# Kernel optimization log

Hardware: AMD Instinct MI355X
Metric: run time of the kernel (lower is better)

The kernel has to match this reference:

```python
import jax, jax.numpy as jnp
import numpy as np

N_NODES = 100000
N_EDGES = 1600000
MUL = 32            # channel multiplicity for every irrep
INV_SQRT_MUL = 1.0 / np.sqrt(32.0)
# path constants: wigner-3j norms (1/sqrt3 for 0x1->1 and 1x1->0, 1/sqrt6 for 1x1->1)
# combined with fan-in path normalization (fan=32 for 0e out, fan=64 for 1o out, 2 paths)
C_DOT = 1.0 / np.sqrt(3.0 * 32.0)
C_SCL = 1.0 / np.sqrt(3.0 * 64.0)
C_CRS = 1.0 / np.sqrt(6.0 * 64.0)


def setup_inputs() -> dict:
    key = jax.random.key(0)
    ks = jax.random.split(key, 12)
    x = jax.random.normal(ks[0], (N_NODES, 128), jnp.float32)
    pos = jax.random.normal(ks[1], (N_NODES, 3), jnp.float32)
    edge_index = jax.random.randint(ks[2], (2, N_EDGES), 0, N_NODES, jnp.int32)
    # o3.Linear(32x0e+32x1o -> 32x0e+32x0e+32x1o): per-irrep channel mixing
    W_node_s = jax.random.normal(ks[3], (32, 64), jnp.float32)   # 0e -> (scalars|gates)
    W_node_v = jax.random.normal(ks[4], (32, 32), jnp.float32)   # 1o -> 1o
    # FullyConnectedTensorProduct(32x0e+32x1o, 1x1o -> 32x0e+32x1o): 3 CG paths
    W_tp_d = jax.random.normal(ks[5], (32, 32), jnp.float32)     # 1o x 1o -> 0e (dot)
    W_tp_s = jax.random.normal(ks[6], (32, 32), jnp.float32)     # 0e x 1o -> 1o
    W_tp_c = jax.random.normal(ks[7], (32, 32), jnp.float32)     # 1o x 1o -> 1o (cross)
    # o3.Linear(32x0e+32x1o -> 32x0e+32x1o)
    W_msg_s = jax.random.normal(ks[8], (32, 32), jnp.float32)
    W_msg_v = jax.random.normal(ks[9], (32, 32), jnp.float32)
    ln_gamma = jnp.ones((128,), jnp.float32)
    ln_beta = jnp.zeros((128,), jnp.float32)
    return {"x": x, "pos": pos, "edge_index": edge_index,
            "W_node_s": W_node_s, "W_node_v": W_node_v,
            "W_tp_d": W_tp_d, "W_tp_s": W_tp_s, "W_tp_c": W_tp_c,
            "W_msg_s": W_msg_s, "W_msg_v": W_msg_v,
            "ln_gamma": ln_gamma, "ln_beta": ln_beta}


def reference(x, pos, edge_index, W_node_s, W_node_v, W_tp_d, W_tp_s, W_tp_c,
              W_msg_s, W_msg_v, ln_gamma, ln_beta):
    N = x.shape[0]
    row, col = edge_index[0], edge_index[1]
    # split node irreps: 32 scalars (0e) | 32 vectors (1o) of dim 3
    s = x[:, :32]                       # [N,32]
    v = x[:, 32:].reshape(-1, 32, 3)    # [N,32,3]
    # lin_node (equivariant linear, path-normalized by 1/sqrt(fan_in)=1/sqrt(32))
    h_s = (s @ W_node_s) * INV_SQRT_MUL                          # [N,64]
    h_v = jnp.einsum('nid,ij->njd', v, W_node_v) * INV_SQRT_MUL  # [N,32,3]
    # Gate: relu scalars, sigmoid gates multiply the gated vectors
    sc = jax.nn.relu(h_s[:, :32])                                # [N,32]
    hv = h_v * jax.nn.sigmoid(h_s[:, 32:])[:, :, None]           # [N,32,3]
    # spherical harmonics l=1, component norm: sqrt(3)*unit vec in e3nn (y,z,x) order
    rel = pos[col] - pos[row]                                    # [E,3]
    unit = rel / jnp.sqrt(jnp.sum(rel * rel, -1, keepdims=True) + 1e-12)
    u = jnp.sqrt(3.0) * unit[:, (1, 2, 0)]                       # [E,3]
    # gather source-node features per edge
    sj = sc[col]                                                 # [E,32]
    vj = hv[col]                                                 # [E,32,3]
    # CG tensor product paths
    dot = jnp.einsum('eid,ed->ei', vj, u)                        # 1o x 1o -> 0e
    crs = jnp.cross(vj, u[:, None, :])                           # 1o x 1o -> 1o
    m0 = (dot @ W_tp_d) * C_DOT                                  # [E,32]
    m1 = (sj @ W_tp_s)[:, :, None] * u[:, None, :] * C_SCL \
         + jnp.einsum('eid,ik->ekd', crs, W_tp_c) * C_CRS        # [E,32,3]
    m = jnp.concatenate([m0, m1.reshape(-1, 96)], -1)            # [E,128]
    # scatter-mean over destination nodes (row)
    deg = jax.ops.segment_sum(jnp.ones_like(row, jnp.float32), row,
                              num_segments=N).clip(1.0)
    mi = jax.ops.segment_sum(m, row, num_segments=N) / deg[:, None]
    # lin_msg
    ms = (mi[:, :32] @ W_msg_s) * INV_SQRT_MUL
    mv = jnp.einsum('nid,ij->njd', mi[:, 32:].reshape(-1, 32, 3),
                    W_msg_v) * INV_SQRT_MUL
    o = jnp.concatenate([ms, mv.reshape(-1, 96)], -1)            # [N,128]
    # LayerNorm over 128 dims (as in the original, affine)
    mu = o.mean(-1, keepdims=True)
    var = o.var(-1, keepdims=True)
    o = (o - mu) / jnp.sqrt(var + 1e-5) * ln_gamma + ln_beta
    return x + o
```

## Files before the change

### kernel.cpp

```cpp
#include <hip/hip_runtime.h>
#include <math.h>


static constexpr float INV_SQRT_MUL = 0.17677669529663687f;
static constexpr float C_DOT = 0.10206207261596575f;
static constexpr float C_SCL = 0.07216878364870322f;
static constexpr float C_CRS = 0.05103103630798288f;
static constexpr float SQRT3 = 1.7320508075688772f;
static constexpr int MAXDEG = 48;
static constexpr int SCAT_B = 2048;
static constexpr int CNT_WORDS = 8 * 16384;

#define WS_ALIGN(x) (((x) + 255) & ~(size_t)255)
#define CIDX(r) ((((r) & 7) << 14) | ((r) >> 3))

__device__ __forceinline__ unsigned short f2bf(float v) {
    unsigned int b = __float_as_uint(v);
    b += 0x7FFFu + ((b >> 16) & 1u);
    return (unsigned short)(b >> 16);
}
__device__ __forceinline__ float bf2f(unsigned short u) {
    return __uint_as_float(((unsigned int)u) << 16);
}

__global__ __launch_bounds__(1024)
void fuse_zero(const float* __restrict__ Wns, const float* __restrict__ Wnv,
               const float* __restrict__ Wtpd, const float* __restrict__ Wtps,
               const float* __restrict__ Wtpc, const float* __restrict__ Wms,
               const float* __restrict__ Wmv, float* __restrict__ Wall,
               int* __restrict__ cnt) {
    int t = threadIdx.x;
    if (blockIdx.x == 0) {
        int i = t >> 5, j = t & 31;
        float a = 0.f, b = 0.f, c = 0.f;
#pragma unroll
        for (int k = 0; k < 32; ++k) {
            a += Wtpd[i * 32 + k] * Wms[k * 32 + j];
            b += Wtps[i * 32 + k] * Wmv[k * 32 + j];
            c += Wtpc[i * 32 + k] * Wmv[k * 32 + j];
        }
        Wall[t]        = a * (C_DOT * INV_SQRT_MUL);
        Wall[1024 + t] = b * (C_SCL * INV_SQRT_MUL);
        Wall[2048 + t] = c * (C_CRS * INV_SQRT_MUL);
        int i2 = t >> 5, k2 = t & 31;
        Wall[3072 + t]        = Wns[k2 * 64 + i2];
        Wall[3072 + 1024 + t] = Wns[k2 * 64 + 32 + i2];
        Wall[5120 + t]        = Wnv[k2 * 32 + i2];
    } else {
        int i = (blockIdx.x - 1) * 1024 + t;
        if (i < CNT_WORDS) cnt[i] = 0;
    }
}

__global__ __launch_bounds__(256)
void scatter(const int* __restrict__ eidx, int* __restrict__ cnt,
             int* __restrict__ slots, int E) {
    int shard = blockIdx.x & 7;
    int tid = (blockIdx.x >> 3) * 256 + threadIdx.x;
    const int SSTRIDE = (SCAT_B / 8) * 256;
    int Q = E >> 2;
    const int4* r4p = (const int4*)eidx;
    const int4* c4p = (const int4*)(eidx + E);
    for (int q = tid; q < Q; q += SSTRIDE) {
        int4 R = r4p[q];
        bool any = ((R.x & 7) == shard) | ((R.y & 7) == shard) |
                   ((R.z & 7) == shard) | ((R.w & 7) == shard);
        if (!any) continue;
        int4 C = c4p[q];
        int rr[4] = {R.x, R.y, R.z, R.w};
        int cc[4] = {C.x, C.y, C.z, C.w};
#pragma unroll
        for (int k = 0; k < 4; ++k) {
            if ((rr[k] & 7) == shard) {
                int p = atomicAdd(&cnt[CIDX(rr[k])], 1);
                if (p < MAXDEG) slots[(size_t)rr[k] * MAXDEG + p] = cc[k];
            }
        }
    }
    for (int e = (Q << 2) + tid; e < E; e += SSTRIDE) {
        int r = eidx[e];
        if ((r & 7) == shard) {
            int c = eidx[E + e];
            int p = atomicAdd(&cnt[CIDX(r)], 1);
            if (p < MAXDEG) slots[(size_t)r * MAXDEG + p] = c;
        }
    }
}

__global__ __launch_bounds__(64)
void node_feat(const float* __restrict__ x, const float* __restrict__ WT,
               ushort4* __restrict__ feat4, int N) {
    __shared__ float buf[64 * 100];
    int l = threadIdx.x;
    int nt = (N + 63) >> 6;
    const float* WnsT = WT;
    const float* WnvT = WT + 2048;
    for (int tile = blockIdx.x; tile < nt; tile += gridDim.x) {
        int B = tile << 6;
        {
            int r0 = l >> 3, cw = (l & 7) * 4;
            for (int j = 0; j < 8; ++j) {
                int row = j * 8 + r0;
                int node = B + row;
                float4 v = make_float4(0.f, 0.f, 0.f, 0.f);
                if (node < N) v = *(const float4*)(x + (size_t)node * 128 + cw);
                *(float4*)(buf + row * 36 + cw) = v;
            }
        }
        __syncthreads();
        float xsv[32];
        {
            const float4* rp = (const float4*)(buf + l * 36);
#pragma unroll
            for (int j = 0; j < 8; ++j) {
                float4 q = rp[j];
                xsv[4 * j] = q.x; xsv[4 * j + 1] = q.y;
                xsv[4 * j + 2] = q.z; xsv[4 * j + 3] = q.w;
            }
        }
        unsigned int scp[16];
        float sig[32];
#pragma unroll 2
        for (int i = 0; i < 32; ++i) {
            float a = 0.f, g = 0.f;
#pragma unroll
            for (int k = 0; k < 32; ++k) {
                a += xsv[k] * WnsT[i * 32 + k];
                g += xsv[k] * WnsT[(32 + i) * 32 + k];
            }
            a = fmaxf(a * INV_SQRT_MUL, 0.f);
            float s = 1.f / (1.f + __expf(-g * INV_SQRT_MUL));
            unsigned short s16 = f2bf(a);
            if ((i & 1) == 0) scp[i >> 1] = s16;
            else scp[i >> 1] |= ((unsigned int)s16) << 16;
            sig[i] = s * INV_SQRT_MUL;
        }
        __syncthreads();
        {
            int r0 = l >> 3, cw = (l & 7) * 4;
            for (int j = 0; j < 24; ++j) {
                int third = j >> 3, j8 = j & 7;
                int row = j8 * 8 + r0;
                int node = B + row;
                int w0 = 32 + third * 32 + cw;
                float4 v = make_float4(0.f, 0.f, 0.f, 0.f);
                if (node < N) v = *(const float4*)(x + (size_t)node * 128 + w0);
                *(float4*)(buf + row * 100 + (w0 - 32)) = v;
            }
        }
        __syncthreads();
        float xv[96];
        {
            const float4* rp = (const float4*)(buf + l * 100);
#pragma unroll
            for (int j = 0; j < 24; ++j) {
                float4 q = rp[j];
                xv[4 * j] = q.x; xv[4 * j + 1] = q.y;
                xv[4 * j + 2] = q.z; xv[4 * j + 3] = q.w;
            }
        }
        int node = B + l;
        bool live = (node < N);
#pragma unroll 2
        for (int i = 0; i < 32; ++i) {
            float o0 = 0.f, o1 = 0.f, o2 = 0.f;
#pragma unroll
            for (int k = 0; k < 32; ++k) {
                float wv = WnvT[i * 32 + k];
                o0 += xv[3 * k + 0] * wv;
                o1 += xv[3 * k + 1] * wv;
                o2 += xv[3 * k + 2] * wv;
            }
            float s = sig[i];
            unsigned int scw = scp[i >> 1];
            ushort4 pk;
            pk.x = (unsigned short)((i & 1) ? (scw >> 16) : (scw & 0xFFFFu));
            pk.y = f2bf(o0 * s); pk.z = f2bf(o1 * s); pk.w = f2bf(o2 * s);
            if (live) feat4[(size_t)node * 32 + i] = pk;
        }
        __syncthreads();
    }
}

template <int U>
__device__ __forceinline__ void agg_chunk(const float4* __restrict__ curow, int j,
    const ushort4* __restrict__ feat4, int lane,
    float& D, float& S0, float& S1, float& S2,
    float& C0, float& C1, float& C2) {
    float4 q[U];
    ushort4 f[U];
#pragma unroll
    for (int k = 0; k < U; ++k) q[k] = curow[j + k];
#pragma unroll
    for (int k = 0; k < U; ++k)
        f[k] = feat4[(size_t)__float_as_int(q[k].w) * 32 + lane];
#pragma unroll
    for (int k = 0; k < U; ++k) {
        float u0 = q[k].x, u1 = q[k].y, u2 = q[k].z;
        float sj = bf2f(f[k].x);
        float h0 = bf2f(f[k].y), h1 = bf2f(f[k].z), h2 = bf2f(f[k].w);
        D  += h0 * u0 + h1 * u1 + h2 * u2;
        S0 += sj * u0; S1 += sj * u1; S2 += sj * u2;
        C0 += h1 * u2 - h2 * u1;
        C1 += h2 * u0 - h0 * u2;
        C2 += h0 * u1 - h1 * u0;
    }
}

__global__ __launch_bounds__(256)
void agg(const float* __restrict__ x, const float* __restrict__ pos,
         const ushort4* __restrict__ feat4, const int* __restrict__ cnt,
         const int* __restrict__ slots, const float* __restrict__ Wall,
         const float* __restrict__ gamma, const float* __restrict__ beta,
         float* __restrict__ out, int N) {
    int t = threadIdx.x;
    int hw = t >> 5, lane = t & 31;
    int n = blockIdx.x * 8 + hw;
    bool live = (n < N);
    int nn = live ? n : 0;

    __shared__ float4 cu[8][MAXDEG];
    __shared__ float4 finA[8][32];
    __shared__ float4 finB[8][32];

    int deg = live ? cnt[CIDX(n)] : 0;
    int c = min(deg, MAXDEG);

    float prx = pos[nn * 3 + 0], pry = pos[nn * 3 + 1], prz = pos[nn * 3 + 2];

    if (lane < c) {
        int col = slots[(size_t)nn * MAXDEG + lane];
        float rx = pos[col * 3 + 0] - prx, ry = pos[col * 3 + 1] - pry, rz = pos[col * 3 + 2] - prz;
        float inv = rsqrtf(rx * rx + ry * ry + rz * rz + 1e-12f) * SQRT3;
        cu[hw][lane] = make_float4(ry * inv, rz * inv, rx * inv, __int_as_float(col));
    }
    if (lane + 32 < c) {
        int col = slots[(size_t)nn * MAXDEG + 32 + lane];
        float rx = pos[col * 3 + 0] - prx, ry = pos[col * 3 + 1] - pry, rz = pos[col * 3 + 2] - prz;
        float inv = rsqrtf(rx * rx + ry * ry + rz * rz + 1e-12f) * SQRT3;
        cu[hw][32 + lane] = make_float4(ry * inv, rz * inv, rx * inv, __int_as_float(col));
    }
    __syncthreads();

    float D = 0.f, S0 = 0.f, S1 = 0.f, S2 = 0.f, C0 = 0.f, C1 = 0.f, C2 = 0.f;
    const float4* curow = cu[hw];
    int j = 0;
    for (; j + 8 <= c; j += 8) agg_chunk<8>(curow, j, feat4, lane, D, S0, S1, S2, C0, C1, C2);
    if (j + 4 <= c) { agg_chunk<4>(curow, j, feat4, lane, D, S0, S1, S2, C0, C1, C2); j += 4; }
    for (; j < c; ++j) agg_chunk<1>(curow, j, feat4, lane, D, S0, S1, S2, C0, C1, C2);

    finA[hw][lane] = make_float4(D, S0, S1, S2);
    finB[hw][lane] = make_float4(C0, C1, C2, 0.f);
    __syncthreads();

    float invdeg = 1.0f / (float)((deg > 0) ? deg : 1);
    float a0 = 0.f, aV0 = 0.f, aV1 = 0.f, aV2 = 0.f;
#pragma unroll 8
    for (int i = 0; i < 32; ++i) {
        float4 a = finA[hw][i];
        float4 b = finB[hw][i];
        float wd = Wall[i * 32 + lane];
        float ws = Wall[1024 + i * 32 + lane];
        float wc = Wall[2048 + i * 32 + lane];
        a0  += a.x * wd;
        aV0 += a.y * ws + b.x * wc;
        aV1 += a.z * ws + b.y * wc;
        aV2 += a.w * ws + b.z * wc;
    }
    float vd = a0 * invdeg;
    float v0 = aV0 * invdeg, v1 = aV1 * invdeg, v2 = aV2 * invdeg;

    float s1 = vd + v0 + v1 + v2;
    float s2 = vd * vd + v0 * v0 + v1 * v1 + v2 * v2;
#pragma unroll
    for (int m = 16; m >= 1; m >>= 1) {
        s1 += __shfl_xor(s1, m);
        s2 += __shfl_xor(s2, m);
    }
    float mu = s1 * (1.f / 128.f);
    float var = s2 * (1.f / 128.f) - mu * mu;
    float rstd = rsqrtf(var + 1e-5f);

    if (live) {
        size_t base = (size_t)n * 128;
        int chv = 32 + lane * 3;
        float xv0 = __builtin_nontemporal_load(&x[base + lane]);
        float xa  = __builtin_nontemporal_load(&x[base + chv + 0]);
        float xb  = __builtin_nontemporal_load(&x[base + chv + 1]);
        float xc  = __builtin_nontemporal_load(&x[base + chv + 2]);
        __builtin_nontemporal_store(xv0 + (vd - mu) * rstd * gamma[lane] + beta[lane], &out[base + lane]);
        __builtin_nontemporal_store(xa + (v0 - mu) * rstd * gamma[chv + 0] + beta[chv + 0], &out[base + chv + 0]);
        __builtin_nontemporal_store(xb + (v1 - mu) * rstd * gamma[chv + 1] + beta[chv + 1], &out[base + chv + 1]);
        __builtin_nontemporal_store(xc + (v2 - mu) * rstd * gamma[chv + 2] + beta[chv + 2], &out[base + chv + 2]);
    }
}

extern "C" void kernel_launch(void* const* d_in, const int* in_sizes, int n_in,
                              void* d_out, int out_size, void* d_ws, size_t ws_size,
                              hipStream_t stream) {
    const float* x     = (const float*)d_in[0];
    const float* pos   = (const float*)d_in[1];
    const int*   eidx  = (const int*)d_in[2];
    const float* Wns   = (const float*)d_in[3];
    const float* Wnv   = (const float*)d_in[4];
    const float* Wtpd  = (const float*)d_in[5];
    const float* Wtps  = (const float*)d_in[6];
    const float* Wtpc  = (const float*)d_in[7];
    const float* Wms   = (const float*)d_in[8];
    const float* Wmv   = (const float*)d_in[9];
    const float* gamma = (const float*)d_in[10];
    const float* beta  = (const float*)d_in[11];
    float* out = (float*)d_out;

    int N = in_sizes[0] / 128;
    int E = in_sizes[2] / 2;

    char* ws = (char*)d_ws;
    size_t off = 0;
    unsigned short* feat = (unsigned short*)(ws + off); off += WS_ALIGN((size_t)N * 128 * 2);
    int*   cnt  = (int*)(ws + off);   off += WS_ALIGN((size_t)CNT_WORDS * 4);
    float* Wall = (float*)(ws + off); off += WS_ALIGN(6144 * 4);
    int*   slots = (int*)(ws + off);

    int zb = 1 + (CNT_WORDS + 1023) / 1024;
    fuse_zero<<<zb, 1024, 0, stream>>>(Wns, Wnv, Wtpd, Wtps, Wtpc, Wms, Wmv, Wall, cnt);
    scatter<<<SCAT_B, 256, 0, stream>>>(eidx, cnt, slots, E);
    int nt = (N + 63) >> 6;
    node_feat<<<nt, 64, 0, stream>>>(x, Wall + 3072, (ushort4*)feat, N);
    agg<<<(N + 7) / 8, 256, 0, stream>>>(x, pos, (const ushort4*)feat, cnt, slots, Wall, gamma, beta, out, N);
}
```

Baseline: 437.5 us.

## Restructure agg to one node per wave with split edges, batch node_feat waves

```diff
diff --git a/kernel.cpp b/kernel.cpp
--- a/kernel.cpp
+++ b/kernel.cpp
@@ -24,32 +24,26 @@
 }
 
 __global__ __launch_bounds__(1024)
-void fuse_zero(const float* __restrict__ Wns, const float* __restrict__ Wnv,
-               const float* __restrict__ Wtpd, const float* __restrict__ Wtps,
-               const float* __restrict__ Wtpc, const float* __restrict__ Wms,
-               const float* __restrict__ Wmv, float* __restrict__ Wall,
-               int* __restrict__ cnt) {
+void fuse_w(const float* __restrict__ Wns, const float* __restrict__ Wnv,
+            const float* __restrict__ Wtpd, const float* __restrict__ Wtps,
+            const float* __restrict__ Wtpc, const float* __restrict__ Wms,
+            const float* __restrict__ Wmv, float* __restrict__ Wall) {
     int t = threadIdx.x;
-    if (blockIdx.x == 0) {
-        int i = t >> 5, j = t & 31;
-        float a = 0.f, b = 0.f, c = 0.f;
-#pragma unroll
-        for (int k = 0; k < 32; ++k) {
-            a += Wtpd[i * 32 + k] * Wms[k * 32 + j];
-            b += Wtps[i * 32 + k] * Wmv[k * 32 + j];
-            c += Wtpc[i * 32 + k] * Wmv[k * 32 + j];
-        }
-        Wall[t]        = a * (C_DOT * INV_SQRT_MUL);
-        Wall[1024 + t] = b * (C_SCL * INV_SQRT_MUL);
-        Wall[2048 + t] = c * (C_CRS * INV_SQRT_MUL);
-        int i2 = t >> 5, k2 = t & 31;
-        Wall[3072 + t]        = Wns[k2 * 64 + i2];
-        Wall[3072 + 1024 + t] = Wns[k2 * 64 + 32 + i2];
-        Wall[5120 + t]        = Wnv[k2 * 32 + i2];
-    } else {
-        int i = (blockIdx.x - 1) * 1024 + t;
-        if (i < CNT_WORDS) cnt[i] = 0;
-    }
+    int i = t >> 5, j = t & 31;
+    float a = 0.f, b = 0.f, c = 0.f;
+#pragma unroll
+    for (int k = 0; k < 32; ++k) {
+        a += Wtpd[i * 32 + k] * Wms[k * 32 + j];
+        b += Wtps[i * 32 + k] * Wmv[k * 32 + j];
+        c += Wtpc[i * 32 + k] * Wmv[k * 32 + j];
+    }
+    Wall[t]        = a * (C_DOT * INV_SQRT_MUL);
+    Wall[1024 + t] = b * (C_SCL * INV_SQRT_MUL);
+    Wall[2048 + t] = c * (C_CRS * INV_SQRT_MUL);
+    int i2 = t >> 5, k2 = t & 31;
+    Wall[3072 + t]        = Wns[k2 * 64 + i2];
+    Wall[3072 + 1024 + t] = Wns[k2 * 64 + 32 + i2];
+    Wall[5120 + t]        = Wnv[k2 * 32 + i2];
 }
 
 __global__ __launch_bounds__(256)
@@ -87,123 +81,83 @@
     }
 }
 
-__global__ __launch_bounds__(64)
+__global__ __launch_bounds__(256)
 void node_feat(const float* __restrict__ x, const float* __restrict__ WT,
                ushort4* __restrict__ feat4, int N) {
-    __shared__ float buf[64 * 100];
-    int l = threadIdx.x;
+    __shared__ float buf[4][64 * 36];
+    int t = threadIdx.x;
+    int wv = t >> 6, l = t & 63;
+    float* bw = buf[wv];
     int nt = (N + 63) >> 6;
+    int tile = blockIdx.x * 4 + wv;
+    if (tile >= nt) return;
+    int B = tile << 6;
+    int r0 = l >> 3, cw = (l & 7) << 2;
     const float* WnsT = WT;
     const float* WnvT = WT + 2048;
-    for (int tile = blockIdx.x; tile < nt; tile += gridDim.x) {
-        int B = tile << 6;
-        {
-            int r0 = l >> 3, cw = (l & 7) * 4;
-            for (int j = 0; j < 8; ++j) {
-                int row = j * 8 + r0;
-                int node = B + row;
-                float4 v = make_float4(0.f, 0.f, 0.f, 0.f);
-                if (node < N) v = *(const float4*)(x + (size_t)node * 128 + cw);
-                *(float4*)(buf + row * 36 + cw) = v;
-            }
-        }
-        __syncthreads();
-        float xsv[32];
-        {
-            const float4* rp = (const float4*)(buf + l * 36);
-#pragma unroll
-            for (int j = 0; j < 8; ++j) {
-                float4 q = rp[j];
-                xsv[4 * j] = q.x; xsv[4 * j + 1] = q.y;
-                xsv[4 * j + 2] = q.z; xsv[4 * j + 3] = q.w;
-            }
-        }
-        unsigned int scp[16];
-        float sig[32];
+
+    auto stage = [&](int w0) {
+#pragma unroll
+        for (int j = 0; j < 8; ++j) {
+            int row = j * 8 + r0;
+            int node = B + row;
+            float4 v = make_float4(0.f, 0.f, 0.f, 0.f);
+            if (node < N) v = *(const float4*)(x + (size_t)node * 128 + w0 + cw);
+            *(float4*)(bw + row * 36 + cw) = v;
+        }
+        __builtin_amdgcn_wave_barrier();
+    };
+    auto readrow = [&](float* dst) {
+        const float4* rp = (const float4*)(bw + l * 36);
+#pragma unroll
+        for (int j = 0; j < 8; ++j) {
+            float4 q = rp[j];
+            dst[4*j] = q.x; dst[4*j+1] = q.y; dst[4*j+2] = q.z; dst[4*j+3] = q.w;
+        }
+        __builtin_amdgcn_wave_barrier();
+    };
+
+    float xs[32];
+    stage(0); readrow(xs);
+    unsigned int scp[16];
+    float sig[32];
 #pragma unroll 2
-        for (int i = 0; i < 32; ++i) {
-            float a = 0.f, g = 0.f;
-#pragma unroll
-            for (int k = 0; k < 32; ++k) {
-                a += xsv[k] * WnsT[i * 32 + k];
-                g += xsv[k] * WnsT[(32 + i) * 32 + k];
-            }
-            a = fmaxf(a * INV_SQRT_MUL, 0.f);
-            float s = 1.f / (1.f + __expf(-g * INV_SQRT_MUL));
-            unsigned short s16 = f2bf(a);
-            if ((i & 1) == 0) scp[i >> 1] = s16;
-            else scp[i >> 1] |= ((unsigned int)s16) << 16;
-            sig[i] = s * INV_SQRT_MUL;
-        }
-        __syncthreads();
-        {
-            int r0 = l >> 3, cw = (l & 7) * 4;
-            for (int j = 0; j < 24; ++j) {
-                int third = j >> 3, j8 = j & 7;
-                int row = j8 * 8 + r0;
-                int node = B + row;
-                int w0 = 32 + third * 32 + cw;
-                float4 v = make_float4(0.f, 0.f, 0.f, 0.f);
-                if (node < N) v = *(const float4*)(x + (size_t)node * 128 + w0);
-                *(float4*)(buf + row * 100 + (w0 - 32)) = v;
-            }
-        }
-        __syncthreads();
-        float xv[96];
-        {
-            const float4* rp = (const float4*)(buf + l * 100);
-#pragma unroll
-            for (int j = 0; j < 24; ++j) {
-                float4 q = rp[j];
-                xv[4 * j] = q.x; xv[4 * j + 1] = q.y;
-                xv[4 * j + 2] = q.z; xv[4 * j + 3] = q.w;
-            }
-        }
-        int node = B + l;
-        bool live = (node < N);
+    for (int i = 0; i < 32; ++i) {
+        float a = 0.f, g = 0.f;
+#pragma unroll
+        for (int k = 0; k < 32; ++k) {
+            a += xs[k] * WnsT[i * 32 + k];
+            g += xs[k] * WnsT[(32 + i) * 32 + k];
+        }
+        a = fmaxf(a * INV_SQRT_MUL, 0.f);
+        float s = 1.f / (1.f + __expf(-g * INV_SQRT_MUL));
+        unsigned short s16 = f2bf(a);
+        if ((i & 1) == 0) scp[i >> 1] = s16;
+        else scp[i >> 1] |= ((unsigned int)s16) << 16;
+        sig[i] = s * INV_SQRT_MUL;
+    }
+    float xv[96];
+    stage(32); readrow(xv);
+    stage(64); readrow(xv + 32);
+    stage(96); readrow(xv + 64);
+    int node = B + l;
+    bool liv = (node < N);
 #pragma unroll 2
-        for (int i = 0; i < 32; ++i) {
-            float o0 = 0.f, o1 = 0.f, o2 = 0.f;
-#pragma unroll
-            for (int k = 0; k < 32; ++k) {
-                float wv = WnvT[i * 32 + k];
-                o0 += xv[3 * k + 0] * wv;
-                o1 += xv[3 * k + 1] * wv;
-                o2 += xv[3 * k + 2] * wv;
-            }
-            float s = sig[i];
-            unsigned int scw = scp[i >> 1];
-            ushort4 pk;
-            pk.x = (unsigned short)((i & 1) ? (scw >> 16) : (scw & 0xFFFFu));
-            pk.y = f2bf(o0 * s); pk.z = f2bf(o1 * s); pk.w = f2bf(o2 * s);
-            if (live) feat4[(size_t)node * 32 + i] = pk;
-        }
-        __syncthreads();
-    }
-}
-
-template <int U>
-__device__ __forceinline__ void agg_chunk(const float4* __restrict__ curow, int j,
-    const ushort4* __restrict__ feat4, int lane,
-    float& D, float& S0, float& S1, float& S2,
-    float& C0, float& C1, float& C2) {
-    float4 q[U];
-    ushort4 f[U];
-#pragma unroll
-    for (int k = 0; k < U; ++k) q[k] = curow[j + k];
-#pragma unroll
-    for (int k = 0; k < U; ++k)
-        f[k] = feat4[(size_t)__float_as_int(q[k].w) * 32 + lane];
-#pragma unroll
-    for (int k = 0; k < U; ++k) {
-        float u0 = q[k].x, u1 = q[k].y, u2 = q[k].z;
-        float sj = bf2f(f[k].x);
-        float h0 = bf2f(f[k].y), h1 = bf2f(f[k].z), h2 = bf2f(f[k].w);
-        D  += h0 * u0 + h1 * u1 + h2 * u2;
-        S0 += sj * u0; S1 += sj * u1; S2 += sj * u2;
-        C0 += h1 * u2 - h2 * u1;
-        C1 += h2 * u0 - h0 * u2;
-        C2 += h0 * u1 - h1 * u0;
+    for (int i = 0; i < 32; ++i) {
+        float o0 = 0.f, o1 = 0.f, o2 = 0.f;
+#pragma unroll
+        for (int k = 0; k < 32; ++k) {
+            float w = WnvT[i * 32 + k];
+            o0 += xv[3 * k + 0] * w;
+            o1 += xv[3 * k + 1] * w;
+            o2 += xv[3 * k + 2] * w;
+        }
+        float s = sig[i];
+        unsigned int scw = scp[i >> 1];
+        ushort4 pk;
+        pk.x = (unsigned short)((i & 1) ? (scw >> 16) : (scw & 0xFFFFu));
+        pk.y = f2bf(o0 * s); pk.z = f2bf(o1 * s); pk.w = f2bf(o2 * s);
+        if (liv) feat4[(size_t)node * 32 + i] = pk;
     }
 }
 
@@ -213,60 +167,89 @@
          const int* __restrict__ slots, const float* __restrict__ Wall,
          const float* __restrict__ gamma, const float* __restrict__ beta,
          float* __restrict__ out, int N) {
+    __shared__ float4 cu[4][MAXDEG];
+    __shared__ float4 finA[4][32];
+    __shared__ float4 finB[4][32];
     int t = threadIdx.x;
-    int hw = t >> 5, lane = t & 31;
-    int n = blockIdx.x * 8 + hw;
+    int wv = t >> 6, lane = t & 63;
+    int ch = lane & 31, slot = lane >> 5;
+    int n = blockIdx.x * 4 + wv;
     bool live = (n < N);
     int nn = live ? n : 0;
-
-    __shared__ float4 cu[8][MAXDEG];
-    __shared__ float4 finA[8][32];
-    __shared__ float4 finB[8][32];
-
-    int deg = live ? cnt[CIDX(n)] : 0;
+    int deg = cnt[CIDX(nn)];
+    if (!live) deg = 0;
     int c = min(deg, MAXDEG);
 
     float prx = pos[nn * 3 + 0], pry = pos[nn * 3 + 1], prz = pos[nn * 3 + 2];
-
     if (lane < c) {
         int col = slots[(size_t)nn * MAXDEG + lane];
         float rx = pos[col * 3 + 0] - prx, ry = pos[col * 3 + 1] - pry, rz = pos[col * 3 + 2] - prz;
         float inv = rsqrtf(rx * rx + ry * ry + rz * rz + 1e-12f) * SQRT3;
-        cu[hw][lane] = make_float4(ry * inv, rz * inv, rx * inv, __int_as_float(col));
-    }
-    if (lane + 32 < c) {
-        int col = slots[(size_t)nn * MAXDEG + 32 + lane];
-        float rx = pos[col * 3 + 0] - prx, ry = pos[col * 3 + 1] - pry, rz = pos[col * 3 + 2] - prz;
-        float inv = rsqrtf(rx * rx + ry * ry + rz * rz + 1e-12f) * SQRT3;
-        cu[hw][32 + lane] = make_float4(ry * inv, rz * inv, rx * inv, __int_as_float(col));
-    }
-    __syncthreads();
-
+        cu[wv][lane] = make_float4(ry * inv, rz * inv, rx * inv, __int_as_float(col << 8));
+    }
+    __builtin_amdgcn_wave_barrier();
+
+    const char* featB = (const char*)feat4;
+    unsigned int ch8 = (unsigned int)ch * 8u;
+    const float4* cuw = cu[wv];
     float D = 0.f, S0 = 0.f, S1 = 0.f, S2 = 0.f, C0 = 0.f, C1 = 0.f, C2 = 0.f;
-    const float4* curow = cu[hw];
-    int j = 0;
-    for (; j + 8 <= c; j += 8) agg_chunk<8>(curow, j, feat4, lane, D, S0, S1, S2, C0, C1, C2);
-    if (j + 4 <= c) { agg_chunk<4>(curow, j, feat4, lane, D, S0, S1, S2, C0, C1, C2); j += 4; }
-    for (; j < c; ++j) agg_chunk<1>(curow, j, feat4, lane, D, S0, S1, S2, C0, C1, C2);
-
-    finA[hw][lane] = make_float4(D, S0, S1, S2);
-    finB[hw][lane] = make_float4(C0, C1, C2, 0.f);
-    __syncthreads();
+
+    auto body = [&](const float4& q, const ushort4& f) {
+        float u0 = q.x, u1 = q.y, u2 = q.z;
+        float sj = bf2f(f.x);
+        float h0 = bf2f(f.y), h1 = bf2f(f.z), h2 = bf2f(f.w);
+        D  += h0 * u0 + h1 * u1 + h2 * u2;
+        S0 += sj * u0; S1 += sj * u1; S2 += sj * u2;
+        C0 += h1 * u2 - h2 * u1;
+        C1 += h2 * u0 - h0 * u2;
+        C2 += h0 * u1 - h1 * u0;
+    };
+
+    int jb = 0;
+    for (; jb + 8 <= c; jb += 8) {
+        float4 q[4]; ushort4 f[4];
+#pragma unroll
+        for (int k = 0; k < 4; ++k) q[k] = cuw[jb + 2 * k + slot];
+#pragma unroll
+        for (int k = 0; k < 4; ++k)
+            f[k] = *(const ushort4*)(featB + (__float_as_uint(q[k].w) + ch8));
+#pragma unroll
+        for (int k = 0; k < 4; ++k) body(q[k], f[k]);
+    }
+    for (int j = jb + slot; j < c; j += 2) {
+        float4 q = cuw[j];
+        ushort4 f = *(const ushort4*)(featB + (__float_as_uint(q.w) + ch8));
+        body(q, f);
+    }
+
+    D  += __shfl_xor(D, 32);
+    S0 += __shfl_xor(S0, 32); S1 += __shfl_xor(S1, 32); S2 += __shfl_xor(S2, 32);
+    C0 += __shfl_xor(C0, 32); C1 += __shfl_xor(C1, 32); C2 += __shfl_xor(C2, 32);
+    if (lane < 32) {
+        finA[wv][ch] = make_float4(D, S0, S1, S2);
+        finB[wv][ch] = make_float4(C0, C1, C2, 0.f);
+    }
+    __builtin_amdgcn_wave_barrier();
 
     float invdeg = 1.0f / (float)((deg > 0) ? deg : 1);
     float a0 = 0.f, aV0 = 0.f, aV1 = 0.f, aV2 = 0.f;
+    int i0 = slot << 4;
 #pragma unroll 8
-    for (int i = 0; i < 32; ++i) {
-        float4 a = finA[hw][i];
-        float4 b = finB[hw][i];
-        float wd = Wall[i * 32 + lane];
-        float ws = Wall[1024 + i * 32 + lane];
-        float wc = Wall[2048 + i * 32 + lane];
+    for (int ii = 0; ii < 16; ++ii) {
+        int i = i0 + ii;
+        float4 a = finA[wv][i];
+        float4 b = finB[wv][i];
+        float wd = Wall[i * 32 + ch];
+        float ws = Wall[1024 + i * 32 + ch];
+        float wc = Wall[2048 + i * 32 + ch];
         a0  += a.x * wd;
         aV0 += a.y * ws + b.x * wc;
         aV1 += a.z * ws + b.y * wc;
         aV2 += a.w * ws + b.z * wc;
     }
+    a0  += __shfl_xor(a0, 32);
+    aV0 += __shfl_xor(aV0, 32); aV1 += __shfl_xor(aV1, 32); aV2 += __shfl_xor(aV2, 32);
+
     float vd = a0 * invdeg;
     float v0 = aV0 * invdeg, v1 = aV1 * invdeg, v2 = aV2 * invdeg;
 
@@ -281,14 +264,14 @@
     float var = s2 * (1.f / 128.f) - mu * mu;
     float rstd = rsqrtf(var + 1e-5f);
 
-    if (live) {
+    if (live && lane < 32) {
         size_t base = (size_t)n * 128;
-        int chv = 32 + lane * 3;
-        float xv0 = __builtin_nontemporal_load(&x[base + lane]);
+        int chv = 32 + ch * 3;
+        float xv0 = __builtin_nontemporal_load(&x[base + ch]);
         float xa  = __builtin_nontemporal_load(&x[base + chv + 0]);
         float xb  = __builtin_nontemporal_load(&x[base + chv + 1]);
         float xc  = __builtin_nontemporal_load(&x[base + chv + 2]);
-        __builtin_nontemporal_store(xv0 + (vd - mu) * rstd * gamma[lane] + beta[lane], &out[base + lane]);
+        __builtin_nontemporal_store(xv0 + (vd - mu) * rstd * gamma[ch] + beta[ch], &out[base + ch]);
         __builtin_nontemporal_store(xa + (v0 - mu) * rstd * gamma[chv + 0] + beta[chv + 0], &out[base + chv + 0]);
         __builtin_nontemporal_store(xb + (v1 - mu) * rstd * gamma[chv + 1] + beta[chv + 1], &out[base + chv + 1]);
         __builtin_nontemporal_store(xc + (v2 - mu) * rstd * gamma[chv + 2] + beta[chv + 2], &out[base + chv + 2]);
@@ -322,10 +305,10 @@
     float* Wall = (float*)(ws + off); off += WS_ALIGN(6144 * 4);
     int*   slots = (int*)(ws + off);
 
-    int zb = 1 + (CNT_WORDS + 1023) / 1024;
-    fuse_zero<<<zb, 1024, 0, stream>>>(Wns, Wnv, Wtpd, Wtps, Wtpc, Wms, Wmv, Wall, cnt);
+    hipMemsetAsync(cnt, 0, (size_t)CNT_WORDS * 4, stream);
+    fuse_w<<<1, 1024, 0, stream>>>(Wns, Wnv, Wtpd, Wtps, Wtpc, Wms, Wmv, Wall);
     scatter<<<SCAT_B, 256, 0, stream>>>(eidx, cnt, slots, E);
     int nt = (N + 63) >> 6;
-    node_feat<<<nt, 64, 0, stream>>>(x, Wall + 3072, (ushort4*)feat, N);
-    agg<<<(N + 7) / 8, 256, 0, stream>>>(x, pos, (const ushort4*)feat, cnt, slots, Wall, gamma, beta, out, N);
-}
+    node_feat<<<(nt + 3) / 4, 256, 0, stream>>>(x, Wall + 3072, (ushort4*)feat, N);
+    agg<<<(N + 3) / 4, 256, 0, stream>>>(x, pos, (const ushort4*)feat, cnt, slots, Wall, gamma, beta, out, N);
+}
```

Measured after the change: 411.2 us. 1.06x faster.
